# Performance work log

Measured on AMD Instinct MI355X. Metric: run time of the kernel, lower is better.

Reference implementation:

```python
import jax, jax.numpy as jnp
import numpy as np

BETA = 0.25
TEMP = 1.0
K = 1024          # codebook_size
DIM = 256         # dim == z_dim


def setup_inputs() -> dict:
    key = jax.random.key(0)
    k1, k2, k3 = jax.random.split(key, 3)
    x = jax.random.normal(k1, (8, 4096, DIM), dtype=jnp.float32)
    # Linear: kaiming_uniform -> sqrt(3/fan_in) * U(-1,1); bias init_bias=0 -> zeros
    W = np.sqrt(3.0 / DIM) * (jax.random.uniform(k2, (DIM, DIM), dtype=jnp.float32) * 2 - 1)
    b = jnp.zeros((DIM,), dtype=jnp.float32)
    # embedding: uniform(-1/K, 1/K)
    emb = jax.random.uniform(k3, (K, DIM), dtype=jnp.float32,
                             minval=-1.0 / K, maxval=1.0 / K)
    return {"x": x, "W": W, "b": b, "emb": emb}


def reference(x, W, b, emb):
    # proj_in: x @ W.T + b
    z = jnp.einsum('bld,od->blo', x, W) + b                     # [B, L, D]
    # squared-L2 distances to codebook (use_norm=False branch)
    dist = (jnp.sum(z * z, axis=-1, keepdims=True)
            + jnp.sum(emb * emb, axis=1)
            - 2.0 * jnp.einsum('bld,nd->bln', z, emb))           # [B, L, K]
    indices = jnp.argmin(dist, axis=-1)                          # [B, L] int
    # ste_prob computed in torch forward (affects grads via one_hot, not outputs)
    quant = emb[indices]                                         # [B, L, D]
    # commitment + codebook loss (training=True)
    loss = (BETA * jnp.mean((jax.lax.stop_gradient(quant) - z) ** 2)
            + jnp.mean((quant - jax.lax.stop_gradient(z)) ** 2))
    # straight-through estimator
    quant = z + jax.lax.stop_gradient(quant - z)
    return quant, indices, loss
```

## Files before the change

### kernel.cpp

```cpp
#include <hip/hip_runtime.h>
#include <hip/hip_bf16.h>

#define TT 32768
#define DD 256
#define KK 1024
#define B_S 5e-4f

typedef __attribute__((ext_vector_type(8)))  short bf16x8;
typedef __attribute__((ext_vector_type(4)))  short bf16x4s;
typedef __attribute__((ext_vector_type(16))) float f32x16;

static inline __device__ short f2bf(float v) {
    __hip_bfloat16 h = __float2bfloat16(v);
    return __builtin_bit_cast(short, h);
}
static inline __device__ float bf2f(short s) {
    __hip_bfloat16 h = __builtin_bit_cast(__hip_bfloat16, s);
    return __bfloat162float(h);
}

static inline __device__ void gload16(const void* g, void* l) {
    __builtin_amdgcn_global_load_lds(
        (const __attribute__((address_space(1))) void*)g,
        (__attribute__((address_space(3))) void*)l,
        16, 0, 0);
}

__global__ void k_ee(const float* __restrict__ emb, float* __restrict__ ee,
                     int* __restrict__ g_nf) {
    if (blockIdx.x == 0 && threadIdx.x == 0) g_nf[0] = 0;
    int n = blockIdx.x * 256 + threadIdx.x;
    if (n >= KK) return;
    const float4* r = (const float4*)(emb + (size_t)n * DD);
    float s = 0.f;
#pragma unroll
    for (int i = 0; i < DD / 4; ++i) {
        float4 v = r[i];
        s += v.x * v.x + v.y * v.y + v.z * v.z + v.w * v.w;
    }
    ee[n] = s;
}

__global__ void k_pack(const float* __restrict__ emb, short* __restrict__ pemb,
                       float4* __restrict__ embP4) {
    int u = blockIdx.x * 256 + threadIdx.x;
    int lane = u & 63;
    int ks  = (u >> 6) & 1, nb = (u >> 7) & 3;
    int kbi = (u >> 9) & 7, nc = (u >> 12) & 7;
    int n = nc * 128 + nb * 32 + (lane & 31);
    int k = kbi * 32 + ks * 16 + (lane >> 5) * 8;
    const float* src = emb + (size_t)n * DD + k;
    float4 v0 = *(const float4*)(src);
    float4 v1 = *(const float4*)(src + 4);
    bf16x8 hb = { f2bf(v0.x), f2bf(v0.y), f2bf(v0.z), f2bf(v0.w),
                  f2bf(v1.x), f2bf(v1.y), f2bf(v1.z), f2bf(v1.w) };
    *(bf16x8*)(pemb + (size_t)u * 8) = hb;
    embP4[(size_t)(k >> 2) * KK + n]       = v0;
    embP4[(size_t)((k >> 2) + 1) * KK + n] = v1;
}

#define PW 40

__launch_bounds__(256, 2)
__global__ void k_proj(const float* __restrict__ x, const float* __restrict__ W,
                       const float* __restrict__ bias, float* __restrict__ z) {
    __shared__ __align__(16) short Ax[3][64 * PW];
    __shared__ __align__(16) short Bw[3][256 * PW];
    const int tid = threadIdx.x;
    const int w = tid >> 6, lane = tid & 63;
    const int l31 = lane & 31, h = lane >> 5;
    const int t0 = blockIdx.x * 64;
    const int wt = (w & 1) * 32;
    const int wc = (w >> 1) * 128;

    f32x16 acc[4];
#pragma unroll
    for (int cb = 0; cb < 4; ++cb)
#pragma unroll
        for (int r = 0; r < 16; ++r) acc[cb][r] = 0.f;

    for (int kb = 0; kb < DD; kb += 32) {
        __syncthreads();
#pragma unroll
        for (int j = 0; j < 2; ++j) {
            int idx = j * 256 + tid, row = idx >> 3, c4 = idx & 7;
            float4 v = *(const float4*)(x + (size_t)(t0 + row) * DD + kb + c4 * 4);
            float e[4] = {v.x, v.y, v.z, v.w};
            bf16x4s s1, s2, s3;
#pragma unroll
            for (int q = 0; q < 4; ++q) {
                short h1 = f2bf(e[q]); float r1 = e[q] - bf2f(h1);
                short h2 = f2bf(r1);   float r2 = r1 - bf2f(h2);
                short h3 = f2bf(r2);
                s1[q] = h1; s2[q] = h2; s3[q] = h3;
            }
            int a = row * PW + c4 * 4;
            *(bf16x4s*)&Ax[0][a] = s1; *(bf16x4s*)&Ax[1][a] = s2; *(bf16x4s*)&Ax[2][a] = s3;
        }
#pragma unroll
        for (int j = 0; j < 8; ++j) {
            int idx = j * 256 + tid, row = idx >> 3, c4 = idx & 7;
            float4 v = *(const float4*)(W + (size_t)row * DD + kb + c4 * 4);
            float e[4] = {v.x, v.y, v.z, v.w};
            bf16x4s s1, s2, s3;
#pragma unroll
            for (int q = 0; q < 4; ++q) {
                short h1 = f2bf(e[q]); float r1 = e[q] - bf2f(h1);
                short h2 = f2bf(r1);   float r2 = r1 - bf2f(h2);
                short h3 = f2bf(r2);
                s1[q] = h1; s2[q] = h2; s3[q] = h3;
            }
            int a = row * PW + c4 * 4;
            *(bf16x4s*)&Bw[0][a] = s1; *(bf16x4s*)&Bw[1][a] = s2; *(bf16x4s*)&Bw[2][a] = s3;
        }
        __syncthreads();
#pragma unroll
        for (int ks = 0; ks < 2; ++ks) {
            int ao = (wt + l31) * PW + ks * 16 + h * 8;
            bf16x8 a1 = *(bf16x8*)&Ax[0][ao];
            bf16x8 a2 = *(bf16x8*)&Ax[1][ao];
            bf16x8 a3 = *(bf16x8*)&Ax[2][ao];
#pragma unroll
            for (int cb = 0; cb < 4; ++cb) {
                int bo = (wc + cb * 32 + l31) * PW + ks * 16 + h * 8;
                bf16x8 b1 = *(bf16x8*)&Bw[0][bo];
                bf16x8 b2 = *(bf16x8*)&Bw[1][bo];
                bf16x8 b3 = *(bf16x8*)&Bw[2][bo];
                acc[cb] = __builtin_amdgcn_mfma_f32_32x32x16_bf16(a1, b3, acc[cb], 0, 0, 0);
                acc[cb] = __builtin_amdgcn_mfma_f32_32x32x16_bf16(a2, b2, acc[cb], 0, 0, 0);
                acc[cb] = __builtin_amdgcn_mfma_f32_32x32x16_bf16(a3, b1, acc[cb], 0, 0, 0);
                acc[cb] = __builtin_amdgcn_mfma_f32_32x32x16_bf16(a1, b2, acc[cb], 0, 0, 0);
                acc[cb] = __builtin_amdgcn_mfma_f32_32x32x16_bf16(a2, b1, acc[cb], 0, 0, 0);
                acc[cb] = __builtin_amdgcn_mfma_f32_32x32x16_bf16(a1, b1, acc[cb], 0, 0, 0);
            }
        }
    }
#pragma unroll
    for (int cb = 0; cb < 4; ++cb) {
        int col = wc + cb * 32 + l31;
        float bc = bias[col];
#pragma unroll
        for (int r = 0; r < 16; ++r) {
            int row = (r & 3) + 8 * (r >> 2) + 4 * h;
            z[(size_t)(t0 + wt + row) * DD + col] = acc[cb][r] + bc;
        }
    }
}

#define SW 264

__launch_bounds__(256, 1)
__global__ void k_screen(const float* __restrict__ z, const short* __restrict__ pemb,
                         const float* __restrict__ ee_g, float* __restrict__ out_idx) {
    __shared__ __align__(16) char smem[65536];
    __shared__ float ee_s[1024];
    __shared__ float zzs[64];

    short* A_s   = (short*)smem;
    float* zpart = (float*)(smem + 33792);
    const int tid = threadIdx.x;
    const int w = tid >> 6, lane = tid & 63;
    const int l31 = lane & 31, h = lane >> 5;
    const int t0 = blockIdx.x * 64;
    const int wr = (w >> 1) * 32;
    const int hw = w & 1;

#pragma unroll
    for (int i = 0; i < 4; ++i) ee_s[i * 256 + tid] = ee_g[i * 256 + tid];

#pragma unroll
    for (int i = 0; i < 16; ++i) {
        int tl = i * 4 + w;
        float4 v = *(const float4*)(z + (size_t)(t0 + tl) * DD + lane * 4);
        float sq = v.x * v.x + v.y * v.y + v.z * v.z + v.w * v.w;
        zpart[tl * 65 + lane] = sq;
        bf16x4s hb = {f2bf(v.x), f2bf(v.y), f2bf(v.z), f2bf(v.w)};
        *(bf16x4s*)&A_s[tl * SW + lane * 4] = hb;
    }
    __syncthreads();

    if (tid < 64) {
        float t_[32];
#pragma unroll
        for (int l = 0; l < 32; ++l) t_[l] = zpart[tid * 65 + l] + zpart[tid * 65 + l + 32];
#pragma unroll
        for (int l = 0; l < 16; ++l) t_[l] = t_[l] + t_[l + 16];
#pragma unroll
        for (int l = 0; l < 8; ++l)  t_[l] = t_[l] + t_[l + 8];
#pragma unroll
        for (int l = 0; l < 4; ++l)  t_[l] = t_[l] + t_[l + 4];
#pragma unroll
        for (int l = 0; l < 2; ++l)  t_[l] = t_[l] + t_[l + 2];
        zzs[tid] = t_[0] + t_[1];
    }

    bf16x8 af[16];
#pragma unroll
    for (int kbi = 0; kbi < 8; ++kbi)
#pragma unroll
        for (int ks = 0; ks < 2; ++ks)
            af[kbi * 2 + ks] = *(bf16x8*)&A_s[(wr + l31) * SW + kbi * 32 + ks * 16 + h * 8];
    __syncthreads();

    float zf[16];
#pragma unroll
    for (int r = 0; r < 16; ++r) zf[r] = zzs[wr + (r & 3) + 8 * (r >> 2) + 4 * h];

    const char* pB = (const char*)pemb;
#pragma unroll
    for (int j = 0; j < 8; ++j)
        gload16(pB + j * 8192 + w * 1024 + lane * 16, smem + j * 4096 + w * 1024);

    float bestv[16], secv[16]; int besti[16];
#pragma unroll
    for (int r = 0; r < 16; ++r) { bestv[r] = 1e30f; secv[r] = 1e30f; besti[r] = 0; }

    for (int ph = 0; ph < 16; ++ph) {
        const int buf = ph & 1;
        char* Bb = smem + buf * 32768;
        asm volatile("s_waitcnt vmcnt(0)" ::: "memory");
        __syncthreads();
        if (ph < 15) {
            const int nn = ph + 1;
            const char* src = pB + (size_t)(nn >> 1) * 65536 + (nn & 1) * 4096;
            char* dst = smem + (buf ^ 1) * 32768;
#pragma unroll
            for (int j = 0; j < 8; ++j)
                gload16(src + j * 8192 + w * 1024 + lane * 16, dst + j * 4096 + w * 1024);
        }
        f32x16 accA, accB;
#pragma unroll
        for (int r = 0; r < 16; ++r) { accA[r] = 0.f; accB[r] = 0.f; }
#pragma unroll
        for (int kbi = 0; kbi < 4; ++kbi) {
            bf16x8 a0b = *(bf16x8*)(Bb + kbi * 4096 + (hw * 2 + 0) * 1024 + lane * 16);
            bf16x8 a1b = *(bf16x8*)(Bb + kbi * 4096 + (hw * 2 + 1) * 1024 + lane * 16);
            bf16x8 b0b = *(bf16x8*)(Bb + (kbi + 4) * 4096 + (hw * 2 + 0) * 1024 + lane * 16);
            bf16x8 b1b = *(bf16x8*)(Bb + (kbi + 4) * 4096 + (hw * 2 + 1) * 1024 + lane * 16);
            accA = __builtin_amdgcn_mfma_f32_32x32x16_bf16(af[kbi * 2 + 0], a0b, accA, 0, 0, 0);
            accB = __builtin_amdgcn_mfma_f32_32x32x16_bf16(af[(kbi + 4) * 2 + 0], b0b, accB, 0, 0, 0);
            accA = __builtin_amdgcn_mfma_f32_32x32x16_bf16(af[kbi * 2 + 1], a1b, accA, 0, 0, 0);
            accB = __builtin_amdgcn_mfma_f32_32x32x16_bf16(af[(kbi + 4) * 2 + 1], b1b, accB, 0, 0, 0);
        }
        {
            int n = (ph >> 1) * 128 + (ph & 1) * 64 + hw * 32 + l31;
            float en = ee_s[n];
#pragma unroll
            for (int r = 0; r < 16; ++r) {
                float u = zf[r] + en;
                float d = accA[r] + accB[r];
                float sc = fmaf(-2.f, d, u);
                if (sc < bestv[r])      { secv[r] = bestv[r]; bestv[r] = sc; besti[r] = n; }
                else if (sc < secv[r])  { secv[r] = sc; }
            }
        }
    }

    __syncthreads();
    float* entV = (float*)smem;
    float* entS = entV + 4224;
    int*   entI = (int*)(entV + 8448);
    const int slot = hw * 32 + l31;
#pragma unroll
    for (int r = 0; r < 16; ++r) {
        int tr = wr + (r & 3) + 8 * (r >> 2) + 4 * h;
        entV[tr * 66 + slot] = bestv[r];
        entS[tr * 66 + slot] = secv[r];
        entI[tr * 66 + slot] = besti[r];
    }
    __syncthreads();
    if (tid < 64) {
        float bv = entV[tid * 66 + 0];
        float sv = entS[tid * 66 + 0];
        int   bi = entI[tid * 66 + 0];
        for (int e = 1; e < 64; ++e) {
            float v  = entV[tid * 66 + e];
            float s2 = entS[tid * 66 + e];
            int   i  = entI[tid * 66 + e];
            float mx = fmaxf(bv, v);
            sv = fminf(fminf(sv, s2), mx);
            if (v < bv || (v == bv && i < bi)) { bv = v; bi = i; }
        }
        float flag = ((sv - bv) < B_S) ? 4096.0f : 0.0f;
        out_idx[t0 + tid] = (float)bi + flag;
    }
}

__global__ void k_compact(const float* __restrict__ out_idx, int* __restrict__ g_nf,
                          int* __restrict__ g_list) {
    __shared__ int wbase[4];
    __shared__ int bbase;
    const int tid = threadIdx.x;
    const int t = blockIdx.x * 256 + tid;
    const int wid = tid >> 6, lane = tid & 63;
    bool fl = out_idx[t] >= 4096.0f;
    unsigned long long m = __ballot(fl);
    if (lane == 0) wbase[wid] = __popcll(m);
    __syncthreads();
    if (tid == 0) {
        int s = 0;
#pragma unroll
        for (int i = 0; i < 4; ++i) { int c = wbase[i]; wbase[i] = s; s += c; }
        bbase = atomicAdd(g_nf, s);
    }
    __syncthreads();
    if (fl) {
        int rank = __popcll(m & ((1ull << lane) - 1ull));
        g_list[bbase + wbase[wid] + rank] = t;
    }
}

#define RB 8

__launch_bounds__(256, 2)
__global__ void k_rescoreT(const float* __restrict__ z, const float4* __restrict__ embP4,
                           const float* __restrict__ ee_g, const int* __restrict__ g_nf,
                           const int* __restrict__ g_list, float* __restrict__ out_idx) {
    __shared__ float zrows[RB][256];
    __shared__ float zz8[RB];
    __shared__ int   toks[RB];
    __shared__ float rv_s[RB][4]; __shared__ int ri_s[RB][4];
    const int tid = threadIdx.x;
    const int w = tid >> 6, lane = tid & 63;
    const int nf = g_nf[0];

    for (int base = blockIdx.x * RB; base < nf; base += gridDim.x * RB) {
        __syncthreads();
        if (tid < RB) toks[tid] = (base + tid < nf) ? g_list[base + tid] : -1;
        __syncthreads();
#pragma unroll
        for (int qq = 0; qq < RB; ++qq) {
            int tok = toks[qq];
            zrows[qq][tid] = (tok >= 0) ? z[(size_t)tok * DD + tid] : 0.f;
        }
        __syncthreads();
        for (int qq = w; qq < RB; qq += 4) {
            float s = 0.f;
#pragma unroll
            for (int k = 0; k < 4; ++k) { float vv = zrows[qq][lane + 64 * k]; s += vv * vv; }
#pragma unroll
            for (int o = 32; o; o >>= 1) s += __shfl_xor(s, o);
            if (lane == 0) zz8[qq] = s;
        }
        __syncthreads();

        float en4[4];
#pragma unroll
        for (int p = 0; p < 4; ++p) en4[p] = ee_g[p * 256 + tid];

        float d[4][RB];
#pragma unroll
        for (int p = 0; p < 4; ++p)
#pragma unroll
            for (int q = 0; q < RB; ++q) d[p][q] = 0.f;

        float4 eA[4], eB[4], zA[RB], zB[RB];
#pragma unroll
        for (int p = 0; p < 4; ++p) eA[p] = embP4[(size_t)0 * KK + p * 256 + tid];
#pragma unroll
        for (int q = 0; q < RB; ++q) zA[q] = *(const float4*)&zrows[q][0];

        for (int k4 = 0; k4 < 64; k4 += 2) {
#pragma unroll
            for (int p = 0; p < 4; ++p) eB[p] = embP4[(size_t)(k4 + 1) * KK + p * 256 + tid];
#pragma unroll
            for (int q = 0; q < RB; ++q) zB[q] = *(const float4*)&zrows[q][(k4 + 1) * 4];
#pragma unroll
            for (int p = 0; p < 4; ++p)
#pragma unroll
                for (int q = 0; q < RB; ++q) {
                    d[p][q] = fmaf(eA[p].x, zA[q].x, d[p][q]);
                    d[p][q] = fmaf(eA[p].y, zA[q].y, d[p][q]);
                    d[p][q] = fmaf(eA[p].z, zA[q].z, d[p][q]);
                    d[p][q] = fmaf(eA[p].w, zA[q].w, d[p][q]);
                }
            if (k4 < 62) {
#pragma unroll
                for (int p = 0; p < 4; ++p) eA[p] = embP4[(size_t)(k4 + 2) * KK + p * 256 + tid];
#pragma unroll
                for (int q = 0; q < RB; ++q) zA[q] = *(const float4*)&zrows[q][(k4 + 2) * 4];
            }
#pragma unroll
            for (int p = 0; p < 4; ++p)
#pragma unroll
                for (int q = 0; q < RB; ++q) {
                    d[p][q] = fmaf(eB[p].x, zB[q].x, d[p][q]);
                    d[p][q] = fmaf(eB[p].y, zB[q].y, d[p][q]);
                    d[p][q] = fmaf(eB[p].z, zB[q].z, d[p][q]);
                    d[p][q] = fmaf(eB[p].w, zB[q].w, d[p][q]);
                }
        }

        float bv[RB]; int bi[RB];
#pragma unroll
        for (int q = 0; q < RB; ++q) { bv[q] = 1e30f; bi[q] = 0; }
#pragma unroll
        for (int p = 0; p < 4; ++p) {
            const int n = p * 256 + tid;
#pragma unroll
            for (int q = 0; q < RB; ++q) {
                float u = zz8[q] + en4[p];
                float s = fmaf(-2.f, d[p][q], u);
                if (s < bv[q]) { bv[q] = s; bi[q] = n; }
            }
        }
        for (int q = 0; q < RB; ++q) {
            float v = bv[q]; int i = bi[q];
#pragma unroll
            for (int o = 1; o < 64; o <<= 1) {
                float ov = __shfl_xor(v, o); int oi = __shfl_xor(i, o);
                if (ov < v || (ov == v && oi < i)) { v = ov; i = oi; }
            }
            if (lane == 0) { rv_s[q][w] = v; ri_s[q][w] = i; }
        }
        __syncthreads();
        if (tid < RB) {
            int tk = toks[tid];
            if (tk >= 0) {
                float fv = rv_s[tid][0]; int fi = ri_s[tid][0];
#pragma unroll
                for (int ww = 1; ww < 4; ++ww) {
                    if (rv_s[tid][ww] < fv || (rv_s[tid][ww] == fv && ri_s[tid][ww] < fi)) {
                        fv = rv_s[tid][ww]; fi = ri_s[tid][ww];
                    }
                }
                out_idx[tk] = (float)fi;
            }
        }
    }
}

__global__ void k_gather(float* __restrict__ zq, const float* __restrict__ emb,
                         const float* __restrict__ out_idx, float* __restrict__ partial) {
    __shared__ float red[4];
    const int tid = threadIdx.x;
    const int t0 = blockIdx.x * 128;
    const int tl = tid >> 1, part = tid & 1;
    int widx = (int)out_idx[t0 + tl];
    widx = min(max(widx, 0), KK - 1);
    const float* erow = emb + (size_t)widx * DD;
    float* qrow = zq + (size_t)(t0 + tl) * DD;
    float lsum = 0.f;
#pragma unroll
    for (int k = 0; k < 32; ++k) {
        int f = part + 2 * k;
        float4 e  = *(const float4*)(erow + f * 4);
        float4 zv = *(const float4*)(qrow + f * 4);
        float dx = e.x - zv.x, dy = e.y - zv.y, dz = e.z - zv.z, dw = e.w - zv.w;
        lsum += dx * dx + dy * dy + dz * dz + dw * dw;
        *(float4*)(qrow + f * 4) = e;
    }
#pragma unroll
    for (int off = 32; off; off >>= 1) lsum += __shfl_down(lsum, off);
    if ((tid & 63) == 0) red[tid >> 6] = lsum;
    __syncthreads();
    if (tid == 0) partial[blockIdx.x] = red[0] + red[1] + red[2] + red[3];
}

__global__ void k_loss(const float* __restrict__ partial, float* __restrict__ out_loss) {
    __shared__ float red[4];
    int tid = threadIdx.x;
    float s = partial[tid];
#pragma unroll
    for (int off = 32; off; off >>= 1) s += __shfl_down(s, off);
    if ((tid & 63) == 0) red[tid >> 6] = s;
    __syncthreads();
    if (tid == 0)
        out_loss[0] = (red[0] + red[1] + red[2] + red[3]) * (1.25f / 8388608.0f);
}

extern "C" void kernel_launch(void* const* d_in, const int* in_sizes, int n_in,
                              void* d_out, int out_size, void* d_ws, size_t ws_size,
                              hipStream_t stream) {
    const float* x   = (const float*)d_in[0];
    const float* W   = (const float*)d_in[1];
    const float* b   = (const float*)d_in[2];
    const float* emb = (const float*)d_in[3];

    float* out   = (float*)d_out;
    float* quant = out;
    float* oidx  = out + (size_t)TT * DD;
    float* oloss = oidx + TT;

    float* wsf     = (float*)d_ws;
    float* ee      = wsf;
    float* partial = wsf + 1024;
    short* pemb    = (short*)(wsf + 1280);
    int*   g_nf    = (int*)(wsf + 132352);
    int*   g_list  = (int*)(wsf + 132353);
    float4* embP4  = (float4*)(wsf + 165124);

    k_ee      <<<KK / 256, 256, 0, stream>>>(emb, ee, g_nf);
    k_pack    <<<128,      256, 0, stream>>>(emb, pemb, embP4);
    k_proj    <<<TT / 64,  256, 0, stream>>>(x, W, b, quant);
    k_screen  <<<TT / 64,  256, 0, stream>>>(quant, pemb, ee, oidx);
    k_compact <<<TT / 256, 256, 0, stream>>>(oidx, g_nf, g_list);
    k_rescoreT<<<512,      256, 0, stream>>>(quant, embP4, ee, g_nf, g_list, oidx);
    k_gather  <<<TT / 128, 256, 0, stream>>>(quant, emb, oidx, partial);
    k_loss    <<<1,        256, 0, stream>>>(partial, oloss);
}
```

Baseline: 259.6 us.

## Pre-split W into MFMA-ready bf16x3 fragments once and load them directly into registers

Adds a k_wpack kernel that splits W into three bf16 parts once per call, laid out in the MFMA fragment order. k_proj now loads those fragments straight into registers instead of having every block re-read fp32 W, split it and stage it through LDS. This removes redundant conversion work and LDS traffic, at the cost of more registers: launch bounds drop from 2 to 1 block per SM and the W fragments are fetched from global or L2 on every k-step. It also adds a sched_barrier and s_setprio around the MFMA loop in k_screen.

```diff
diff --git a/kernel.cpp b/kernel.cpp
--- a/kernel.cpp
+++ b/kernel.cpp
@@ -59,19 +59,45 @@
     embP4[(size_t)((k >> 2) + 1) * KK + n] = v1;
 }
 
+__global__ void k_wpack(const float* __restrict__ W, short* __restrict__ Wp) {
+    int idx = blockIdx.x * 256 + threadIdx.x;
+    int lane = idx & 63;
+    int ks = (idx >> 6) & 1, cb = (idx >> 7) & 3;
+    int g  = (idx >> 9) & 1, kb = (idx >> 10) & 7;
+    int row = g * 128 + cb * 32 + (lane & 31);
+    int col = kb * 32 + ks * 16 + (lane >> 5) * 8;
+    const float* src = W + (size_t)row * DD + col;
+    float4 v0 = *(const float4*)(src);
+    float4 v1 = *(const float4*)(src + 4);
+    float e[8] = {v0.x, v0.y, v0.z, v0.w, v1.x, v1.y, v1.z, v1.w};
+    bf16x8 s1, s2, s3;
+#pragma unroll
+    for (int q = 0; q < 8; ++q) {
+        short h1 = f2bf(e[q]); float r1 = e[q] - bf2f(h1);
+        short h2 = f2bf(r1);   float r2 = r1 - bf2f(h2);
+        short h3 = f2bf(r2);
+        s1[q] = h1; s2[q] = h2; s3[q] = h3;
+    }
+    size_t c0 = ((((size_t)kb * 3 + 0) * 2 + g) * 4 + cb) * 2 + ks;
+    size_t c1 = ((((size_t)kb * 3 + 1) * 2 + g) * 4 + cb) * 2 + ks;
+    size_t c2 = ((((size_t)kb * 3 + 2) * 2 + g) * 4 + cb) * 2 + ks;
+    *(bf16x8*)(Wp + c0 * 512 + lane * 8) = s1;
+    *(bf16x8*)(Wp + c1 * 512 + lane * 8) = s2;
+    *(bf16x8*)(Wp + c2 * 512 + lane * 8) = s3;
+}
+
 #define PW 40
 
-__launch_bounds__(256, 2)
-__global__ void k_proj(const float* __restrict__ x, const float* __restrict__ W,
+__launch_bounds__(256, 1)
+__global__ void k_proj(const float* __restrict__ x, const short* __restrict__ Wp,
                        const float* __restrict__ bias, float* __restrict__ z) {
     __shared__ __align__(16) short Ax[3][64 * PW];
-    __shared__ __align__(16) short Bw[3][256 * PW];
     const int tid = threadIdx.x;
     const int w = tid >> 6, lane = tid & 63;
     const int l31 = lane & 31, h = lane >> 5;
     const int t0 = blockIdx.x * 64;
     const int wt = (w & 1) * 32;
-    const int wc = (w >> 1) * 128;
+    const int g  = (w >> 1);
 
     f32x16 acc[4];
 #pragma unroll
@@ -79,12 +105,22 @@
 #pragma unroll
         for (int r = 0; r < 16; ++r) acc[cb][r] = 0.f;
 
-    for (int kb = 0; kb < DD; kb += 32) {
-        __syncthreads();
+    for (int kb8 = 0; kb8 < 8; ++kb8) {
+        __syncthreads();
+        bf16x8 wb[2][4][3];
+#pragma unroll
+        for (int ks = 0; ks < 2; ++ks)
+#pragma unroll
+            for (int cb = 0; cb < 4; ++cb)
+#pragma unroll
+                for (int s = 0; s < 3; ++s) {
+                    size_t c = ((((size_t)kb8 * 3 + s) * 2 + g) * 4 + cb) * 2 + ks;
+                    wb[ks][cb][s] = *(const bf16x8*)(Wp + c * 512 + lane * 8);
+                }
 #pragma unroll
         for (int j = 0; j < 2; ++j) {
             int idx = j * 256 + tid, row = idx >> 3, c4 = idx & 7;
-            float4 v = *(const float4*)(x + (size_t)(t0 + row) * DD + kb + c4 * 4);
+            float4 v = *(const float4*)(x + (size_t)(t0 + row) * DD + kb8 * 32 + c4 * 4);
             float e[4] = {v.x, v.y, v.z, v.w};
             bf16x4s s1, s2, s3;
 #pragma unroll
@@ -97,22 +133,6 @@
             int a = row * PW + c4 * 4;
             *(bf16x4s*)&Ax[0][a] = s1; *(bf16x4s*)&Ax[1][a] = s2; *(bf16x4s*)&Ax[2][a] = s3;
         }
-#pragma unroll
-        for (int j = 0; j < 8; ++j) {
-            int idx = j * 256 + tid, row = idx >> 3, c4 = idx & 7;
-            float4 v = *(const float4*)(W + (size_t)row * DD + kb + c4 * 4);
-            float e[4] = {v.x, v.y, v.z, v.w};
-            bf16x4s s1, s2, s3;
-#pragma unroll
-            for (int q = 0; q < 4; ++q) {
-                short h1 = f2bf(e[q]); float r1 = e[q] - bf2f(h1);
-                short h2 = f2bf(r1);   float r2 = r1 - bf2f(h2);
-                short h3 = f2bf(r2);
-                s1[q] = h1; s2[q] = h2; s3[q] = h3;
-            }
-            int a = row * PW + c4 * 4;
-            *(bf16x4s*)&Bw[0][a] = s1; *(bf16x4s*)&Bw[1][a] = s2; *(bf16x4s*)&Bw[2][a] = s3;
-        }
         __syncthreads();
 #pragma unroll
         for (int ks = 0; ks < 2; ++ks) {
@@ -122,10 +142,9 @@
             bf16x8 a3 = *(bf16x8*)&Ax[2][ao];
 #pragma unroll
             for (int cb = 0; cb < 4; ++cb) {
-                int bo = (wc + cb * 32 + l31) * PW + ks * 16 + h * 8;
-                bf16x8 b1 = *(bf16x8*)&Bw[0][bo];
-                bf16x8 b2 = *(bf16x8*)&Bw[1][bo];
-                bf16x8 b3 = *(bf16x8*)&Bw[2][bo];
+                bf16x8 b1 = wb[ks][cb][0];
+                bf16x8 b2 = wb[ks][cb][1];
+                bf16x8 b3 = wb[ks][cb][2];
                 acc[cb] = __builtin_amdgcn_mfma_f32_32x32x16_bf16(a1, b3, acc[cb], 0, 0, 0);
                 acc[cb] = __builtin_amdgcn_mfma_f32_32x32x16_bf16(a2, b2, acc[cb], 0, 0, 0);
                 acc[cb] = __builtin_amdgcn_mfma_f32_32x32x16_bf16(a3, b1, acc[cb], 0, 0, 0);
@@ -137,7 +156,7 @@
     }
 #pragma unroll
     for (int cb = 0; cb < 4; ++cb) {
-        int col = wc + cb * 32 + l31;
+        int col = g * 128 + cb * 32 + l31;
         float bc = bias[col];
 #pragma unroll
         for (int r = 0; r < 16; ++r) {
@@ -228,9 +247,11 @@
             for (int j = 0; j < 8; ++j)
                 gload16(src + j * 8192 + w * 1024 + lane * 16, dst + j * 4096 + w * 1024);
         }
+        __builtin_amdgcn_sched_barrier(0);
         f32x16 accA, accB;
 #pragma unroll
         for (int r = 0; r < 16; ++r) { accA[r] = 0.f; accB[r] = 0.f; }
+        __builtin_amdgcn_s_setprio(1);
 #pragma unroll
         for (int kbi = 0; kbi < 4; ++kbi) {
             bf16x8 a0b = *(bf16x8*)(Bb + kbi * 4096 + (hw * 2 + 0) * 1024 + lane * 16);
@@ -242,6 +263,7 @@
             accA = __builtin_amdgcn_mfma_f32_32x32x16_bf16(af[kbi * 2 + 1], a1b, accA, 0, 0, 0);
             accB = __builtin_amdgcn_mfma_f32_32x32x16_bf16(af[(kbi + 4) * 2 + 1], b1b, accB, 0, 0, 0);
         }
+        __builtin_amdgcn_s_setprio(0);
         {
             int n = (ph >> 1) * 128 + (ph & 1) * 64 + hw * 32 + l31;
             float en = ee_s[n];
@@ -489,10 +511,12 @@
     int*   g_nf    = (int*)(wsf + 132352);
     int*   g_list  = (int*)(wsf + 132353);
     float4* embP4  = (float4*)(wsf + 165124);
+    short* Wp      = (short*)(wsf + 427268);
 
     k_ee      <<<KK / 256, 256, 0, stream>>>(emb, ee, g_nf);
     k_pack    <<<128,      256, 0, stream>>>(emb, pemb, embP4);
-    k_proj    <<<TT / 64,  256, 0, stream>>>(x, W, b, quant);
+    k_wpack   <<<32,       256, 0, stream>>>(W, Wp);
+    k_proj    <<<TT / 64,  256, 0, stream>>>(x, Wp, b, quant);
     k_screen  <<<TT / 64,  256, 0, stream>>>(quant, pemb, ee, oidx);
     k_compact <<<TT / 256, 256, 0, stream>>>(oidx, g_nf, g_list);
     k_rescoreT<<<512,      256, 0, stream>>>(quant, embP4, ee, g_nf, g_list, oidx);
```

Measured after the change: 264.7 us. About the same (+2.0%).
